# Kernel optimization log

Hardware: AMD Instinct MI355X
Metric: run time of the kernel (lower is better)

Reference implementation:

```python
import jax, jax.numpy as jnp
import numpy as np

N_NODES = 100000
N_EDGES = 1600000
NODE_F = 64
EDGE_F = 16
OUT_F = 64


def setup_inputs() -> dict:
    key = jax.random.key(0)
    k1, k2, k3, k4, k5 = jax.random.split(key, 5)
    feat = jax.random.normal(k1, (N_NODES, NODE_F), dtype=jnp.float32)
    edge_feats = jax.random.normal(k2, (N_EDGES, EDGE_F), dtype=jnp.float32)
    src = jax.random.randint(k3, (N_EDGES,), 0, N_NODES, dtype=jnp.int64)
    dst = jax.random.randint(k4, (N_EDGES,), 0, N_NODES, dtype=jnp.int64)
    # xavier-normal-ish weight, zero bias (matches reset_parameters)
    fan_in, fan_out = NODE_F + EDGE_F, OUT_F
    std = (2.0 / (fan_in + fan_out)) ** 0.5
    weight = jax.random.normal(k5, (fan_in, fan_out), dtype=jnp.float32) * std
    bias = jnp.zeros((OUT_F,), dtype=jnp.float32)
    return {"feat": feat, "edge_feats": edge_feats, "src": src, "dst": dst,
            "weight": weight, "bias": bias}


def reference(feat, edge_feats, src, dst, weight, bias):
    N = feat.shape[0]
    # in-degree based symmetric-ish norm: pow(clamp(in_deg,1), -0.5)
    deg = jax.ops.segment_sum(jnp.ones(dst.shape, dtype=feat.dtype), dst,
                              num_segments=N)
    norm = jnp.clip(deg, 1.0) ** -0.5  # [N]
    norm = norm[:, None]
    # sum over incoming edges of concat([edge_feats, h_src]).
    # sum of concat == concat of sums, so aggregate each part separately
    # (avoids materializing the per-edge concat).
    sum_e = jax.ops.segment_sum(edge_feats, dst, num_segments=N)  # [N, E_F]
    sum_h = jax.ops.segment_sum(feat[src], dst, num_segments=N)   # [N, NODE_F]
    sum_f = jnp.concatenate([sum_e, sum_h], axis=-1)              # [N, E_F+NODE_F]
    out = (sum_f * norm) @ weight
    out = out * norm + bias
    return jax.nn.selu(out)
```

## Files before the change

### kernel.cpp

```cpp
#include <hip/hip_runtime.h>
#include <math.h>

#define N_NODES 100000
#define N_EDGES 1600000
#define OUT_F   64
#define SCAN_B  1024
#define NBLK    ((N_NODES + SCAN_B - 1) / SCAN_B)

#define EQ4      (N_EDGES / 4)
#define HIST_BLK ((EQ4 + 255) / 256)
#define GEMM_BLK 512

typedef __attribute__((ext_vector_type(8))) short bf16x8;
typedef __attribute__((ext_vector_type(4))) float f32x4;

__device__ __forceinline__ unsigned short f2bf_rne(float f) {
    unsigned u = __float_as_uint(f);
    return (unsigned short)((u + 0x7fffu + ((u >> 16) & 1u)) >> 16);
}
__device__ __forceinline__ float bf2f(unsigned short h) {
    return __uint_as_float((unsigned)h << 16);
}

__global__ __launch_bounds__(256) void prep_hist(
    const float* __restrict__ feat, const float* __restrict__ weight,
    const int* __restrict__ dst,
    unsigned short* __restrict__ G, unsigned* __restrict__ deg_i,
    unsigned short* __restrict__ pos)
{
    int tid = threadIdx.x;

    if (blockIdx.x < HIST_BLK) {
        int q = blockIdx.x * 256 + tid;
        if (q >= EQ4) return;
        int4 d = ((const int4*)dst)[q];
        ushort4 p;
        p.x = (unsigned short)atomicAdd(&deg_i[d.x], 1u);
        p.y = (unsigned short)atomicAdd(&deg_i[d.y], 1u);
        p.z = (unsigned short)atomicAdd(&deg_i[d.z], 1u);
        p.w = (unsigned short)atomicAdd(&deg_i[d.w], 1u);
        ((ushort4*)pos)[q] = p;
        return;
    }

    int gb = (int)blockIdx.x - HIST_BLK;
    int wv = tid >> 6, ln = tid & 63;
    int li = ln & 15, lk = ln >> 4;

    bf16x8 Whi[4][2], Wlo[4][2];
    #pragma unroll
    for (int it = 0; it < 4; ++it)
        #pragma unroll
        for (int kb = 0; kb < 2; ++kb)
            #pragma unroll
            for (int j = 0; j < 8; ++j) {
                float w = weight[(16 + kb * 32 + lk * 8 + j) * 64 + it * 16 + li];
                unsigned short h = f2bf_rne(w);
                Whi[it][kb][j] = (short)h;
                Wlo[it][kb][j] = (short)f2bf_rne(w - bf2f(h));
            }

    const int tiles = N_NODES / 16;
    for (int tile = gb * 4 + wv; tile < tiles; tile += GEMM_BLK * 4) {
        int n = tile * 16 + li;
        const float* fr = feat + (size_t)n * 64 + lk * 8;

        bf16x8 Bhi[2], Blo[2];
        #pragma unroll
        for (int kb = 0; kb < 2; ++kb) {
            float4 v0 = *(const float4*)(fr + kb * 32);
            float4 v1 = *(const float4*)(fr + kb * 32 + 4);
            float vv[8] = {v0.x, v0.y, v0.z, v0.w, v1.x, v1.y, v1.z, v1.w};
            #pragma unroll
            for (int j = 0; j < 8; ++j) {
                unsigned short h = f2bf_rne(vv[j]);
                Bhi[kb][j] = (short)h;
                Blo[kb][j] = (short)f2bf_rne(vv[j] - bf2f(h));
            }
        }

        f32x4 acc[4] = {{0.f,0.f,0.f,0.f},{0.f,0.f,0.f,0.f},
                        {0.f,0.f,0.f,0.f},{0.f,0.f,0.f,0.f}};
        #pragma unroll
        for (int kb = 0; kb < 2; ++kb)
            #pragma unroll
            for (int it = 0; it < 4; ++it) {
                acc[it] = __builtin_amdgcn_mfma_f32_16x16x32_bf16(Whi[it][kb], Bhi[kb], acc[it], 0, 0, 0);
                acc[it] = __builtin_amdgcn_mfma_f32_16x16x32_bf16(Wlo[it][kb], Bhi[kb], acc[it], 0, 0, 0);
                acc[it] = __builtin_amdgcn_mfma_f32_16x16x32_bf16(Whi[it][kb], Blo[kb], acc[it], 0, 0, 0);
            }

        #pragma unroll
        for (int it = 0; it < 4; ++it) {
            ushort4 o;
            o.x = f2bf_rne(acc[it][0]);
            o.y = f2bf_rne(acc[it][1]);
            o.z = f2bf_rne(acc[it][2]);
            o.w = f2bf_rne(acc[it][3]);
            *(ushort4*)(G + (size_t)n * 64 + it * 16 + lk * 4) = o;
        }
    }
}

__global__ __launch_bounds__(SCAN_B) void scanA(
    const unsigned* __restrict__ deg_i, unsigned* __restrict__ bsum)
{
    __shared__ unsigned ws[16];
    int i = blockIdx.x * SCAN_B + threadIdx.x;
    unsigned v = (i < N_NODES) ? deg_i[i] : 0u;
    #pragma unroll
    for (int o = 32; o; o >>= 1) v += __shfl_down(v, o);
    if ((threadIdx.x & 63) == 0) ws[threadIdx.x >> 6] = v;
    __syncthreads();
    if (threadIdx.x < 16) {
        unsigned t = ws[threadIdx.x];
        #pragma unroll
        for (int o = 8; o; o >>= 1) t += __shfl_down(t, o);
        if (threadIdx.x == 0) bsum[blockIdx.x] = t;
    }
}

__global__ __launch_bounds__(SCAN_B) void scanC(
    const unsigned* __restrict__ deg_i, const unsigned* __restrict__ bsum,
    unsigned* __restrict__ off)
{
    __shared__ unsigned ws[17];
    int t = threadIdx.x;

    if (t < 64) {
        unsigned a = 0u;
        for (int j = t; j < (int)blockIdx.x; j += 64) a += bsum[j];
        #pragma unroll
        for (int o = 32; o; o >>= 1) a += __shfl_down(a, o);
        if (t == 0) ws[16] = a;
    }

    int i = blockIdx.x * SCAN_B + t;
    unsigned v = (i < N_NODES) ? deg_i[i] : 0u;
    unsigned x = v;
    #pragma unroll
    for (int o = 1; o < 64; o <<= 1) {
        unsigned u = __shfl_up(x, o);
        if ((t & 63) >= o) x += u;
    }
    if ((t & 63) == 63) ws[t >> 6] = x;
    __syncthreads();
    if (t < 16) {
        unsigned y = ws[t];
        #pragma unroll
        for (int o = 1; o < 16; o <<= 1) {
            unsigned u = __shfl_up(y, o);
            if (t >= o) y += u;
        }
        ws[t] = y;
    }
    __syncthreads();
    unsigned base = ws[16] + ((t >> 6) ? ws[(t >> 6) - 1] : 0u);
    unsigned excl = base + x - v;
    if (i < N_NODES) off[i] = excl;
    if (i == N_NODES - 1) off[N_NODES] = excl + v;
}

__global__ __launch_bounds__(256) void fill_kernel(
    const int* __restrict__ src, const int* __restrict__ dst,
    const unsigned short* __restrict__ pos, const unsigned* __restrict__ off,
    unsigned long long* __restrict__ csr_pack)
{
    int q = blockIdx.x * 256 + threadIdx.x;
    if (q >= EQ4) return;
    int4 s = ((const int4*)src)[q];
    int4 d = ((const int4*)dst)[q];
    ushort4 p = ((const ushort4*)pos)[q];
    unsigned e = (unsigned)q * 4u;
    csr_pack[off[d.x] + (unsigned)p.x] =
        (unsigned long long)(unsigned)s.x | ((unsigned long long)(e + 0u) << 32);
    csr_pack[off[d.y] + (unsigned)p.y] =
        (unsigned long long)(unsigned)s.y | ((unsigned long long)(e + 1u) << 32);
    csr_pack[off[d.z] + (unsigned)p.z] =
        (unsigned long long)(unsigned)s.z | ((unsigned long long)(e + 2u) << 32);
    csr_pack[off[d.w] + (unsigned)p.w] =
        (unsigned long long)(unsigned)s.w | ((unsigned long long)(e + 3u) << 32);
}

__global__ __launch_bounds__(256) void gather_out(
    const unsigned short* __restrict__ G,
    const float* __restrict__ edge_feats,
    const unsigned long long* __restrict__ csr_pack,
    const unsigned* __restrict__ off,
    const float* __restrict__ weight,
    const float* __restrict__ bias,
    float* __restrict__ out)
{
    int tid = threadIdx.x;
    int wv = tid >> 6, ln = tid & 63;

    float We[16];
    #pragma unroll
    for (int k = 0; k < 16; ++k) We[k] = weight[k * 64 + ln];
    float b = bias[ln];

    const float SC = 1.0507009873554805f;
    const float AL = 1.6732632423543772f;

    int n = blockIdx.x * 4 + wv;
    if (n >= N_NODES) return;

    unsigned start = off[n], end = off[n + 1];
    float norm2 = 1.0f / fmaxf((float)(end - start), 1.0f);

    const int gq = ln >> 4;
    const int eq = ln >> 2;

    float gh4[4] = {0.f, 0.f, 0.f, 0.f};
    float ae4[4] = {0.f, 0.f, 0.f, 0.f};

    const ushort4* __restrict__ Gv = (const ushort4*)G;

    for (unsigned base = start; base < end; base += 64u) {
        unsigned m = min(64u, end - base);
        unsigned lo = 0u, hi = 0u;
        if ((unsigned)ln < m) {
            unsigned long long pk = csr_pack[base + (unsigned)ln];
            lo = (unsigned)pk;
            hi = (unsigned)(pk >> 32);
        }

        for (unsigned i = 0; i < m; i += 8u) {
            unsigned i0 = i + (unsigned)gq, i1 = i0 + 4u;
            unsigned s0 = __shfl(lo, (int)min(i0, m - 1u));
            unsigned s1 = __shfl(lo, (int)min(i1, m - 1u));
            ushort4 q0 = {0,0,0,0}, q1 = {0,0,0,0};
            if (i0 < m) q0 = Gv[(size_t)s0 * 16u + (unsigned)(ln & 15)];
            if (i1 < m) q1 = Gv[(size_t)s1 * 16u + (unsigned)(ln & 15)];
            gh4[0] += __uint_as_float((unsigned)q0.x << 16) + __uint_as_float((unsigned)q1.x << 16);
            gh4[1] += __uint_as_float((unsigned)q0.y << 16) + __uint_as_float((unsigned)q1.y << 16);
            gh4[2] += __uint_as_float((unsigned)q0.z << 16) + __uint_as_float((unsigned)q1.z << 16);
            gh4[3] += __uint_as_float((unsigned)q0.w << 16) + __uint_as_float((unsigned)q1.w << 16);
        }

        for (unsigned i = 0; i < m; i += 16u) {
            unsigned ie = i + (unsigned)eq;
            unsigned e0 = __shfl(hi, (int)min(ie, m - 1u));
            if (ie < m) {
                float4 v = *(const float4*)(edge_feats + (size_t)e0 * 16u + (unsigned)(ln & 3) * 4u);
                ae4[0] += v.x; ae4[1] += v.y; ae4[2] += v.z; ae4[3] += v.w;
            }
        }
    }

    #pragma unroll
    for (int c = 0; c < 4; ++c) {
        gh4[c] += __shfl_xor(gh4[c], 16);
        gh4[c] += __shfl_xor(gh4[c], 32);
        ae4[c] += __shfl_xor(ae4[c], 4);
        ae4[c] += __shfl_xor(ae4[c], 8);
        ae4[c] += __shfl_xor(ae4[c], 16);
        ae4[c] += __shfl_xor(ae4[c], 32);
    }
    int srcl = ln >> 2;
    float r0 = __shfl(gh4[0], srcl);
    float r1 = __shfl(gh4[1], srcl);
    float r2 = __shfl(gh4[2], srcl);
    float r3 = __shfl(gh4[3], srcl);
    int c = ln & 3;
    float gh = (c & 2) ? ((c & 1) ? r3 : r2) : ((c & 1) ? r1 : r0);

    float acc = gh;
    #pragma unroll
    for (int k = 0; k < 16; ++k)
        acc = fmaf(__shfl(ae4[k & 3], k >> 2), We[k], acc);

    float o = acc * norm2 + b;
    out[(size_t)n * 64u + ln] = (o > 0.f) ? SC * o : SC * AL * expm1f(o);
}

extern "C" void kernel_launch(void* const* d_in, const int* in_sizes, int n_in,
                              void* d_out, int out_size, void* d_ws, size_t ws_size,
                              hipStream_t stream) {
    const float* feat       = (const float*)d_in[0];
    const float* edge_feats = (const float*)d_in[1];
    const int*   src        = (const int*)d_in[2];
    const int*   dst        = (const int*)d_in[3];
    const float* weight     = (const float*)d_in[4];
    const float* bias       = (const float*)d_in[5];
    float* out = (float*)d_out;

    unsigned long long* csr_pack = (unsigned long long*)d_ws;
    unsigned short* G   = (unsigned short*)(csr_pack + N_EDGES);
    unsigned short* pos = G + (size_t)N_NODES * 64;
    unsigned* deg_i = (unsigned*)(pos + N_EDGES);
    unsigned* off   = deg_i + N_NODES;
    unsigned* bsum  = off + N_NODES + 1;

    hipMemsetAsync(deg_i, 0, N_NODES * sizeof(unsigned), stream);
    prep_hist<<<dim3(HIST_BLK + GEMM_BLK), dim3(256), 0, stream>>>(
        feat, weight, dst, G, deg_i, pos);
    scanA<<<dim3(NBLK), dim3(SCAN_B), 0, stream>>>(deg_i, bsum);
    scanC<<<dim3(NBLK), dim3(SCAN_B), 0, stream>>>(deg_i, bsum, off);
    fill_kernel<<<dim3(HIST_BLK), dim3(256), 0, stream>>>(
        src, dst, pos, off, csr_pack);
    gather_out<<<dim3((N_NODES + 3) / 4), dim3(256), 0, stream>>>(
        G, edge_feats, csr_pack, off, weight, bias, out);
}
```

Baseline: 355.6 us.

## Fold block sums into histogram, move GEMM into fill, use fast SELU math

The histogram kernel now also accumulates per-1024-node block totals in shared memory and adds them atomically to bsum, which removes the separate scanA reduction launch. The feature-projection GEMM blocks move from the histogram kernel into the CSR fill kernel, so the fill's scattered writes run alongside MFMA work. The memset is widened to zero bsum as well. In the output stage, the exact reciprocal and expm1f are replaced by the hardware rcp and __expf(o)-1, which trade some accuracy near zero for fewer instructions.

```diff
diff --git a/kernel.cpp b/kernel.cpp
--- a/kernel.cpp
+++ b/kernel.cpp
@@ -22,17 +22,17 @@
     return __uint_as_float((unsigned)h << 16);
 }
 
-__global__ __launch_bounds__(256) void prep_hist(
-    const float* __restrict__ feat, const float* __restrict__ weight,
-    const int* __restrict__ dst,
-    unsigned short* __restrict__ G, unsigned* __restrict__ deg_i,
-    unsigned short* __restrict__ pos)
-{
+__global__ __launch_bounds__(256) void hist(
+    const int* __restrict__ dst, unsigned* __restrict__ deg_i,
+    unsigned short* __restrict__ pos, unsigned* __restrict__ bsum)
+{
+    __shared__ unsigned lbin[NBLK];
     int tid = threadIdx.x;
-
-    if (blockIdx.x < HIST_BLK) {
-        int q = blockIdx.x * 256 + tid;
-        if (q >= EQ4) return;
+    if (tid < NBLK) lbin[tid] = 0u;
+    __syncthreads();
+
+    int q = blockIdx.x * 256 + tid;
+    if (q < EQ4) {
         int4 d = ((const int4*)dst)[q];
         ushort4 p;
         p.x = (unsigned short)atomicAdd(&deg_i[d.x], 1u);
@@ -40,6 +40,83 @@
         p.z = (unsigned short)atomicAdd(&deg_i[d.z], 1u);
         p.w = (unsigned short)atomicAdd(&deg_i[d.w], 1u);
         ((ushort4*)pos)[q] = p;
+        atomicAdd(&lbin[d.x >> 10], 1u);
+        atomicAdd(&lbin[d.y >> 10], 1u);
+        atomicAdd(&lbin[d.z >> 10], 1u);
+        atomicAdd(&lbin[d.w >> 10], 1u);
+    }
+    __syncthreads();
+    if (tid < NBLK) {
+        unsigned v = lbin[tid];
+        if (v) atomicAdd(&bsum[tid], v);
+    }
+}
+
+__global__ __launch_bounds__(SCAN_B) void scanC(
+    const unsigned* __restrict__ deg_i, const unsigned* __restrict__ bsum,
+    unsigned* __restrict__ off)
+{
+    __shared__ unsigned ws[17];
+    int t = threadIdx.x;
+
+    if (t < 64) {
+        unsigned a = 0u;
+        for (int j = t; j < (int)blockIdx.x; j += 64) a += bsum[j];
+        #pragma unroll
+        for (int o = 32; o; o >>= 1) a += __shfl_down(a, o);
+        if (t == 0) ws[16] = a;
+    }
+
+    int i = blockIdx.x * SCAN_B + t;
+    unsigned v = (i < N_NODES) ? deg_i[i] : 0u;
+    unsigned x = v;
+    #pragma unroll
+    for (int o = 1; o < 64; o <<= 1) {
+        unsigned u = __shfl_up(x, o);
+        if ((t & 63) >= o) x += u;
+    }
+    if ((t & 63) == 63) ws[t >> 6] = x;
+    __syncthreads();
+    if (t < 16) {
+        unsigned y = ws[t];
+        #pragma unroll
+        for (int o = 1; o < 16; o <<= 1) {
+            unsigned u = __shfl_up(y, o);
+            if (t >= o) y += u;
+        }
+        ws[t] = y;
+    }
+    __syncthreads();
+    unsigned base = ws[16] + ((t >> 6) ? ws[(t >> 6) - 1] : 0u);
+    unsigned excl = base + x - v;
+    if (i < N_NODES) off[i] = excl;
+    if (i == N_NODES - 1) off[N_NODES] = excl + v;
+}
+
+__global__ __launch_bounds__(256) void fill_gemm(
+    const int* __restrict__ src, const int* __restrict__ dst,
+    const unsigned short* __restrict__ pos, const unsigned* __restrict__ off,
+    unsigned long long* __restrict__ csr_pack,
+    const float* __restrict__ feat, const float* __restrict__ weight,
+    unsigned short* __restrict__ G)
+{
+    int tid = threadIdx.x;
+
+    if (blockIdx.x < HIST_BLK) {
+        int q = blockIdx.x * 256 + tid;
+        if (q >= EQ4) return;
+        int4 s = ((const int4*)src)[q];
+        int4 d = ((const int4*)dst)[q];
+        ushort4 p = ((const ushort4*)pos)[q];
+        unsigned e = (unsigned)q * 4u;
+        csr_pack[off[d.x] + (unsigned)p.x] =
+            (unsigned long long)(unsigned)s.x | ((unsigned long long)(e + 0u) << 32);
+        csr_pack[off[d.y] + (unsigned)p.y] =
+            (unsigned long long)(unsigned)s.y | ((unsigned long long)(e + 1u) << 32);
+        csr_pack[off[d.z] + (unsigned)p.z] =
+            (unsigned long long)(unsigned)s.z | ((unsigned long long)(e + 2u) << 32);
+        csr_pack[off[d.w] + (unsigned)p.w] =
+            (unsigned long long)(unsigned)s.w | ((unsigned long long)(e + 3u) << 32);
         return;
     }
 
@@ -102,86 +179,6 @@
     }
 }
 
-__global__ __launch_bounds__(SCAN_B) void scanA(
-    const unsigned* __restrict__ deg_i, unsigned* __restrict__ bsum)
-{
-    __shared__ unsigned ws[16];
-    int i = blockIdx.x * SCAN_B + threadIdx.x;
-    unsigned v = (i < N_NODES) ? deg_i[i] : 0u;
-    #pragma unroll
-    for (int o = 32; o; o >>= 1) v += __shfl_down(v, o);
-    if ((threadIdx.x & 63) == 0) ws[threadIdx.x >> 6] = v;
-    __syncthreads();
-    if (threadIdx.x < 16) {
-        unsigned t = ws[threadIdx.x];
-        #pragma unroll
-        for (int o = 8; o; o >>= 1) t += __shfl_down(t, o);
-        if (threadIdx.x == 0) bsum[blockIdx.x] = t;
-    }
-}
-
-__global__ __launch_bounds__(SCAN_B) void scanC(
-    const unsigned* __restrict__ deg_i, const unsigned* __restrict__ bsum,
-    unsigned* __restrict__ off)
-{
-    __shared__ unsigned ws[17];
-    int t = threadIdx.x;
-
-    if (t < 64) {
-        unsigned a = 0u;
-        for (int j = t; j < (int)blockIdx.x; j += 64) a += bsum[j];
-        #pragma unroll
-        for (int o = 32; o; o >>= 1) a += __shfl_down(a, o);
-        if (t == 0) ws[16] = a;
-    }
-
-    int i = blockIdx.x * SCAN_B + t;
-    unsigned v = (i < N_NODES) ? deg_i[i] : 0u;
-    unsigned x = v;
-    #pragma unroll
-    for (int o = 1; o < 64; o <<= 1) {
-        unsigned u = __shfl_up(x, o);
-        if ((t & 63) >= o) x += u;
-    }
-    if ((t & 63) == 63) ws[t >> 6] = x;
-    __syncthreads();
-    if (t < 16) {
-        unsigned y = ws[t];
-        #pragma unroll
-        for (int o = 1; o < 16; o <<= 1) {
-            unsigned u = __shfl_up(y, o);
-            if (t >= o) y += u;
-        }
-        ws[t] = y;
-    }
-    __syncthreads();
-    unsigned base = ws[16] + ((t >> 6) ? ws[(t >> 6) - 1] : 0u);
-    unsigned excl = base + x - v;
-    if (i < N_NODES) off[i] = excl;
-    if (i == N_NODES - 1) off[N_NODES] = excl + v;
-}
-
-__global__ __launch_bounds__(256) void fill_kernel(
-    const int* __restrict__ src, const int* __restrict__ dst,
-    const unsigned short* __restrict__ pos, const unsigned* __restrict__ off,
-    unsigned long long* __restrict__ csr_pack)
-{
-    int q = blockIdx.x * 256 + threadIdx.x;
-    if (q >= EQ4) return;
-    int4 s = ((const int4*)src)[q];
-    int4 d = ((const int4*)dst)[q];
-    ushort4 p = ((const ushort4*)pos)[q];
-    unsigned e = (unsigned)q * 4u;
-    csr_pack[off[d.x] + (unsigned)p.x] =
-        (unsigned long long)(unsigned)s.x | ((unsigned long long)(e + 0u) << 32);
-    csr_pack[off[d.y] + (unsigned)p.y] =
-        (unsigned long long)(unsigned)s.y | ((unsigned long long)(e + 1u) << 32);
-    csr_pack[off[d.z] + (unsigned)p.z] =
-        (unsigned long long)(unsigned)s.z | ((unsigned long long)(e + 2u) << 32);
-    csr_pack[off[d.w] + (unsigned)p.w] =
-        (unsigned long long)(unsigned)s.w | ((unsigned long long)(e + 3u) << 32);
-}
-
 __global__ __launch_bounds__(256) void gather_out(
     const unsigned short* __restrict__ G,
     const float* __restrict__ edge_feats,
@@ -206,7 +203,7 @@
     if (n >= N_NODES) return;
 
     unsigned start = off[n], end = off[n + 1];
-    float norm2 = 1.0f / fmaxf((float)(end - start), 1.0f);
+    float norm2 = __builtin_amdgcn_rcpf(fmaxf((float)(end - start), 1.0f));
 
     const int gq = ln >> 4;
     const int eq = ln >> 2;
@@ -271,7 +268,7 @@
         acc = fmaf(__shfl(ae4[k & 3], k >> 2), We[k], acc);
 
     float o = acc * norm2 + b;
-    out[(size_t)n * 64u + ln] = (o > 0.f) ? SC * o : SC * AL * expm1f(o);
+    out[(size_t)n * 64u + ln] = (o > 0.f) ? SC * o : SC * AL * (__expf(o) - 1.0f);
 }
 
 extern "C" void kernel_launch(void* const* d_in, const int* in_sizes, int n_in,
@@ -292,13 +289,11 @@
     unsigned* off   = deg_i + N_NODES;
     unsigned* bsum  = off + N_NODES + 1;
 
-    hipMemsetAsync(deg_i, 0, N_NODES * sizeof(unsigned), stream);
-    prep_hist<<<dim3(HIST_BLK + GEMM_BLK), dim3(256), 0, stream>>>(
-        feat, weight, dst, G, deg_i, pos);
-    scanA<<<dim3(NBLK), dim3(SCAN_B), 0, stream>>>(deg_i, bsum);
+    hipMemsetAsync(deg_i, 0, (size_t)(N_NODES + N_NODES + 1 + NBLK) * sizeof(unsigned), stream);
+    hist<<<dim3(HIST_BLK), dim3(256), 0, stream>>>(dst, deg_i, pos, bsum);
     scanC<<<dim3(NBLK), dim3(SCAN_B), 0, stream>>>(deg_i, bsum, off);
-    fill_kernel<<<dim3(HIST_BLK), dim3(256), 0, stream>>>(
-        src, dst, pos, off, csr_pack);
+    fill_gemm<<<dim3(HIST_BLK + GEMM_BLK), dim3(256), 0, stream>>>(
+        src, dst, pos, off, csr_pack, feat, weight, G);
     gather_out<<<dim3((N_NODES + 3) / 4), dim3(256), 0, stream>>>(
         G, edge_feats, csr_pack, off, weight, bias, out);
 }
```

Result: slower. 377.3 us (+6.1%).
